# Performance work log

Measured on AMD Instinct MI355X. Metric: run time of the kernel, lower is better.

The kernel has to match this reference:

```python
import jax, jax.numpy as jnp
import numpy as np

N = 50000          # nodes
E = 640000         # edges (before self-loops)
DIM_FEATS = 128
DIM_H = 32
HEADS1 = 8
NUM_CLASS = 16
NEG_SLOPE_ATT = 0.2   # PyG GATv2Conv default negative_slope
NEG_SLOPE_OUT = 0.01  # F.leaky_relu default


def setup_inputs() -> dict:
    key = jax.random.key(0)
    ks = jax.random.split(key, 12)
    s = 0.1
    x = jax.random.normal(ks[0], (N, DIM_FEATS), dtype=jnp.float32)
    edge_index = jax.random.randint(ks[1], (2, E), 0, N, dtype=jnp.int32)
    # GATv2Conv layer 1: dim_feats -> dim_h per head, 8 heads, concat
    W1l = jax.random.normal(ks[2], (DIM_FEATS, HEADS1 * DIM_H), dtype=jnp.float32) * s
    W1r = jax.random.normal(ks[3], (DIM_FEATS, HEADS1 * DIM_H), dtype=jnp.float32) * s
    att1 = jax.random.normal(ks[4], (HEADS1, DIM_H), dtype=jnp.float32) * s
    b1 = jnp.zeros((HEADS1 * DIM_H,), dtype=jnp.float32)
    # GATv2Conv layer 2: 256 -> num_class, 1 head, concat=False
    W2l = jax.random.normal(ks[5], (HEADS1 * DIM_H, NUM_CLASS), dtype=jnp.float32) * s
    W2r = jax.random.normal(ks[6], (HEADS1 * DIM_H, NUM_CLASS), dtype=jnp.float32) * s
    att2 = jax.random.normal(ks[7], (1, NUM_CLASS), dtype=jnp.float32) * s
    b2 = jnp.zeros((NUM_CLASS,), dtype=jnp.float32)
    return {"x": x, "edge_index": edge_index, "W1l": W1l, "W1r": W1r,
            "att1": att1, "b1": b1, "W2l": W2l, "W2r": W2r,
            "att2": att2, "b2": b2}


def _segment_softmax(scores, seg, num_segments):
    # scores: [E, H], seg: [E] destination node ids
    m = jax.ops.segment_max(scores, seg, num_segments=num_segments)  # [N, H]
    e = jnp.exp(scores - m[seg])
    denom = jax.ops.segment_sum(e, seg, num_segments=num_segments)   # [N, H]
    return e / (denom[seg] + 1e-16)


def _gatv2_layer(x, src, dst, Wl, Wr, att, bias, heads, out_ch, concat):
    n = x.shape[0]
    xl = (x @ Wl).reshape(n, heads, out_ch)  # source transform
    xr = (x @ Wr).reshape(n, heads, out_ch)  # target transform
    # per-edge GATv2 score: a^T LeakyReLU(xl[j] + xr[i])
    e = jax.nn.leaky_relu(xl[src] + xr[dst], negative_slope=NEG_SLOPE_ATT)  # [E,H,F]
    alpha = jnp.einsum('ehf,hf->eh', e, att)                                # [E,H]
    alpha = _segment_softmax(alpha, dst, n)
    msg = xl[src] * alpha[:, :, None]                                       # [E,H,F]
    out = jax.ops.segment_sum(msg, dst, num_segments=n)                     # [N,H,F]
    out = out.reshape(n, heads * out_ch) if concat else out.mean(axis=1)
    return out + bias


def reference(x, edge_index, W1l, W1r, att1, b1, W2l, W2r, att2, b2):
    # add_self_loops=True (PyG GATv2Conv default)
    loop = jnp.arange(N, dtype=edge_index.dtype)
    src = jnp.concatenate([edge_index[0], loop])
    dst = jnp.concatenate([edge_index[1], loop])
    # eval mode: all dropouts are identity
    h = _gatv2_layer(x, src, dst, W1l, W1r, att1, b1, HEADS1, DIM_H, concat=True)
    h = jax.nn.elu(h)
    h = _gatv2_layer(h, src, dst, W2l, W2r, att2, b2, 1, NUM_CLASS, concat=False)
    return jax.nn.leaky_relu(h, negative_slope=NEG_SLOPE_OUT)
```

## Files before the change

kernel.cpp:

```cpp
#include <hip/hip_runtime.h>
#include <math.h>

#define NN 50000
#define E0 640000
#define ET 690000
#define F1 128
#define D1 256
#define C2 16
#define NB 196
#define MPAD 50048
#define PADK 136
#define LOG2E 1.4426950408889634f
#define NBK1 782

typedef _Float16 f16x8 __attribute__((ext_vector_type(8)));
typedef _Float16 h2 __attribute__((ext_vector_type(2)));
typedef __attribute__((ext_vector_type(4))) float f32x4;

__device__ __forceinline__ unsigned short f2h(float f) {
  union { _Float16 h; unsigned short u; } c;
  c.h = (_Float16)f;
  return c.u;
}
__device__ __forceinline__ float h2f(unsigned short u) {
  union { unsigned short u; _Float16 h; } c; c.u = u; return (float)c.h;
}
__device__ __forceinline__ h2 u2h2(unsigned u) {
  union { unsigned u; h2 h; } c; c.u = u; return c.h;
}
__device__ __forceinline__ unsigned h22u(h2 h) {
  union { h2 h; unsigned u; } c; c.h = h; return c.u;
}

__global__ __launch_bounds__(256) void k_prep(
    const float* __restrict__ Wl, const float* __restrict__ Wr,
    const float* __restrict__ W2l, const float* __restrict__ W2r,
    const int* __restrict__ ei,
    unsigned short* __restrict__ wt, unsigned short* __restrict__ wt2,
    int* __restrict__ deg) {
  const int b = blockIdx.x;
  if (b < 256) {
    int tid = b * 256 + threadIdx.x;
    int n = tid >> 7, k = tid & 127;
    float v = (n < 256) ? Wl[k * 256 + n] : Wr[k * 256 + (n - 256)];
    wt[tid] = f2h(v);
  } else if (b < 288) {
    int tid = (b - 256) * 256 + threadIdx.x;
    int n = tid >> 8, k = tid & 255;
    float v = (n < 16) ? W2l[k * 16 + n] : W2r[k * 16 + (n - 16)];
    wt2[tid] = f2h(v);
  } else {
    int e = (b - 288) * 256 + threadIdx.x;
    if (e >= ET) return;
    int d = (e < E0) ? ei[E0 + e] : (e - E0);
    atomicAdd(&deg[d], 1);
  }
}

__global__ __launch_bounds__(256) void k_gemm1m(
    const float* __restrict__ x, const unsigned short* __restrict__ wt,
    unsigned short* __restrict__ xlh, unsigned short* __restrict__ xrh) {
  __shared__ unsigned short Al[128 * PADK];
  __shared__ unsigned short Bl[128 * PADK];
  const int t = threadIdx.x;
  const int m0 = blockIdx.x * 128;
  const int n0 = blockIdx.y * 128;
  {
    const int r = t >> 4;
    const int c = (t & 15) * 8;
#pragma unroll
    for (int p = 0; p < 8; ++p) {
      const int row = r + p * 16;
      const int rg = m0 + row;
      const float* xp = &x[(size_t)(rg < NN ? rg : NN - 1) * F1 + c];
      float4 lo = *(const float4*)xp;
      float4 hi = *(const float4*)(xp + 4);
      h2 q0 = h2{(_Float16)lo.x, (_Float16)lo.y};
      h2 q1 = h2{(_Float16)lo.z, (_Float16)lo.w};
      h2 q2 = h2{(_Float16)hi.x, (_Float16)hi.y};
      h2 q3 = h2{(_Float16)hi.z, (_Float16)hi.w};
      uint4 st; st.x = h22u(q0); st.y = h22u(q1); st.z = h22u(q2); st.w = h22u(q3);
      *(uint4*)&Al[row * PADK + c] = st;
      *(float4*)&Bl[row * PADK + c] = *(const float4*)&wt[(size_t)(n0 + row) * F1 + c];
    }
  }
  __syncthreads();
  const int wave = t >> 6, lane = t & 63;
  const int mw = (wave >> 1) * 64, nw = (wave & 1) * 64;
  const int fr = lane & 15, fq = lane >> 4;
  f32x4 acc[4][4] = {};
#pragma unroll
  for (int ks = 0; ks < 4; ++ks) {
    const int ko = ks * 32 + fq * 8;
    f16x8 a[4], b[4];
#pragma unroll
    for (int i = 0; i < 4; ++i)
      a[i] = *(const f16x8*)&Al[(mw + i * 16 + fr) * PADK + ko];
#pragma unroll
    for (int j = 0; j < 4; ++j)
      b[j] = *(const f16x8*)&Bl[(nw + j * 16 + fr) * PADK + ko];
#pragma unroll
    for (int i = 0; i < 4; ++i)
#pragma unroll
      for (int j = 0; j < 4; ++j)
        acc[i][j] = __builtin_amdgcn_mfma_f32_16x16x32_f16(a[i], b[j], acc[i][j], 0, 0, 0);
  }
  unsigned short* outp = (n0 < 256) ? xlh : xrh;
  const int cb = (n0 & 255) + nw + fr;
#pragma unroll
  for (int j = 0; j < 4; ++j) {
    const int col = cb + j * 16;
    const int head = col >> 5, f = col & 31;
    unsigned short* hp = outp + (size_t)head * NN * 32 + f;
#pragma unroll
    for (int i = 0; i < 4; ++i) {
      const int gm0 = m0 + mw + i * 16 + fq * 4;
#pragma unroll
      for (int r = 0; r < 4; ++r) {
        const int gm = gm0 + r;
        if (gm < NN) hp[(size_t)gm * 32] = f2h(acc[i][j][r]);
      }
    }
  }
}

__global__ __launch_bounds__(256) void k_scan_part(const int* __restrict__ deg,
                                                   int* __restrict__ part) {
  int i = blockIdx.x * 256 + threadIdx.x;
  int v = (i < NN) ? deg[i] : 0;
  v += __shfl_xor(v, 1);  v += __shfl_xor(v, 2);  v += __shfl_xor(v, 4);
  v += __shfl_xor(v, 8);  v += __shfl_xor(v, 16); v += __shfl_xor(v, 32);
  __shared__ int w[4];
  if ((threadIdx.x & 63) == 0) w[threadIdx.x >> 6] = v;
  __syncthreads();
  if (threadIdx.x == 0) part[blockIdx.x] = w[0] + w[1] + w[2] + w[3];
}

__global__ __launch_bounds__(256) void k_scan_apply(int* __restrict__ deg,
                                                    const int* __restrict__ part,
                                                    int* __restrict__ offs) {
  __shared__ int lds[256];
  __shared__ int red[4];
  const int b = blockIdx.x, t = threadIdx.x;
  const int i = b * 256 + t;
  int v = (i < NN) ? deg[i] : 0;
  lds[t] = v;
  int pp = 0;
  for (int j = t; j < b; j += 256) pp += part[j];
  pp += __shfl_xor(pp, 1);  pp += __shfl_xor(pp, 2);  pp += __shfl_xor(pp, 4);
  pp += __shfl_xor(pp, 8);  pp += __shfl_xor(pp, 16); pp += __shfl_xor(pp, 32);
  if ((t & 63) == 0) red[t >> 6] = pp;
  __syncthreads();
  const int prefix = red[0] + red[1] + red[2] + red[3];
  for (int off = 1; off < 256; off <<= 1) {
    int u = (t >= off) ? lds[t - off] : 0;
    __syncthreads();
    lds[t] += u;
    __syncthreads();
  }
  int excl = prefix + lds[t] - v;
  if (i < NN) { offs[i] = excl; deg[i] = excl; }
  if (b == NB - 1 && t == 255) offs[NN] = prefix + lds[255];
}

__global__ void k_scatter(const int* __restrict__ ei, int* __restrict__ cur,
                          unsigned short* __restrict__ csr) {
  int e = blockIdx.x * 256 + threadIdx.x;
  if (e >= ET) return;
  int s, d;
  if (e < E0) { s = ei[e]; d = ei[E0 + e]; } else { s = d = e - E0; }
  int pos = atomicAdd(&cur[d], 1);
  csr[pos] = (unsigned short)s;
}

__global__ __launch_bounds__(256) void k_agg1(
    const unsigned short* __restrict__ xlh, const unsigned short* __restrict__ xrh,
    unsigned short* __restrict__ hb,
    const int* __restrict__ offs, const unsigned short* __restrict__ csr,
    const float* __restrict__ att, const float* __restrict__ b1) {
  const int b = blockIdx.x;
  const int head = b & 7;
  const int wave = threadIdx.x >> 6;
  const int lane = threadIdx.x & 63;
  const int g = lane >> 2;
  const int j4 = lane & 3;
  const int n = (b >> 3) * 64 + wave * 16 + g;
  const bool valid = n < NN;
  const int colh = j4 * 8;
  const int col = head * 32 + colh;
  const unsigned short* xlhead = xlh + (size_t)head * NN * 32;

  const int nc = valid ? n : 0;
  const uint4 xru = *(const uint4*)&xrh[((size_t)head * NN + nc) * 32 + colh];
  h2 xr2[4];
  xr2[0] = u2h2(xru.x); xr2[1] = u2h2(xru.y);
  xr2[2] = u2h2(xru.z); xr2[3] = u2h2(xru.w);
  float at8[8];
  *(float4*)&at8[0] = *(const float4*)&att[col];
  *(float4*)&at8[4] = *(const float4*)&att[col + 4];
  h2 ath6[4], ath4[4];
#pragma unroll
  for (int j = 0; j < 4; ++j) {
    ath6[j] = h2{(_Float16)(at8[2 * j] * (0.6f * LOG2E)),
                 (_Float16)(at8[2 * j + 1] * (0.6f * LOG2E))};
    ath4[j] = h2{(_Float16)(at8[2 * j] * (0.4f * LOG2E)),
                 (_Float16)(at8[2 * j + 1] * (0.4f * LOG2E))};
  }
  float l = 0.f;
  h2 acc2[4] = {h2{0, 0}, h2{0, 0}, h2{0, 0}, h2{0, 0}};
  const int beg = valid ? offs[n] : 0;
  const int fin = valid ? offs[n + 1] : 0;

  auto score = [&](const h2* xh) -> float {
    float cv = 0.f, ca = 0.f;
#pragma unroll
    for (int j = 0; j < 4; ++j) {
      h2 v = xh[j] + xr2[j];
      h2 a = u2h2(h22u(v) & 0x7FFF7FFFu);
      cv = __builtin_amdgcn_fdot2(v, ath6[j], cv, false);
      ca = __builtin_amdgcn_fdot2(a, ath4[j], ca, false);
    }
    float c = cv + ca;
    c += __shfl_xor(c, 1);
    c += __shfl_xor(c, 2);
    return c;
  };

  int idx = beg;
  for (; idx + 1 < fin; idx += 2) {
    const int s0 = csr[idx], s1 = csr[idx + 1];
    const uint4 w0 = *(const uint4*)&xlhead[(size_t)s0 * 32 + colh];
    const uint4 w1 = *(const uint4*)&xlhead[(size_t)s1 * 32 + colh];
    h2 xh0[4], xh1[4];
    xh0[0] = u2h2(w0.x); xh0[1] = u2h2(w0.y); xh0[2] = u2h2(w0.z); xh0[3] = u2h2(w0.w);
    xh1[0] = u2h2(w1.x); xh1[1] = u2h2(w1.y); xh1[2] = u2h2(w1.z); xh1[3] = u2h2(w1.w);
    const float c0 = score(xh0);
    const float c1 = score(xh1);
    const float p0 = exp2f(c0), p1 = exp2f(c1);
    l += p0 + p1;
    const _Float16 p0h = (_Float16)p0, p1h = (_Float16)p1;
    const h2 p02 = h2{p0h, p0h}, p12 = h2{p1h, p1h};
#pragma unroll
    for (int j = 0; j < 4; ++j) acc2[j] += p02 * xh0[j] + p12 * xh1[j];
  }
  if (idx < fin) {
    const int s0 = csr[idx];
    const uint4 w0 = *(const uint4*)&xlhead[(size_t)s0 * 32 + colh];
    h2 xh0[4];
    xh0[0] = u2h2(w0.x); xh0[1] = u2h2(w0.y); xh0[2] = u2h2(w0.z); xh0[3] = u2h2(w0.w);
    const float c0 = score(xh0);
    const float p0 = exp2f(c0);
    l += p0;
    const _Float16 p0h = (_Float16)p0;
    const h2 p02 = h2{p0h, p0h};
#pragma unroll
    for (int j = 0; j < 4; ++j) acc2[j] += p02 * xh0[j];
  }
  if (valid) {
    const float rl = 1.f / (l + 1e-16f);
    float b8[8], o[8];
    *(float4*)&b8[0] = *(const float4*)&b1[col];
    *(float4*)&b8[4] = *(const float4*)&b1[col + 4];
#pragma unroll
    for (int j = 0; j < 4; ++j) {
      o[2 * j]     = (float)acc2[j][0] * rl + b8[2 * j];
      o[2 * j + 1] = (float)acc2[j][1] * rl + b8[2 * j + 1];
    }
#pragma unroll
    for (int k = 0; k < 8; ++k) o[k] = o[k] > 0.f ? o[k] : expm1f(o[k]);
    ushort4 p;
    p.x = f2h(o[0]); p.y = f2h(o[1]); p.z = f2h(o[2]); p.w = f2h(o[3]);
    ushort4 q;
    q.x = f2h(o[4]); q.y = f2h(o[5]); q.z = f2h(o[6]); q.w = f2h(o[7]);
    uint4 packed;
    packed.x = *(unsigned*)&p.x; packed.y = *(unsigned*)&p.z;
    packed.z = *(unsigned*)&q.x; packed.w = *(unsigned*)&q.z;
    *(uint4*)&hb[(size_t)n * D1 + col] = packed;
  }
}

__global__ __launch_bounds__(256) void k_gemm2m(
    const unsigned short* __restrict__ hb, const unsigned short* __restrict__ wt2,
    unsigned short* __restrict__ h2lh, float* __restrict__ h2r) {
  const int t = threadIdx.x;
  const int wave = t >> 6, lane = t & 63;
  const int fr = lane & 15, fq = lane >> 4;
  const int m0 = blockIdx.x * 128 + wave * 32;
  f32x4 acc[2][2] = {};
#pragma unroll
  for (int ks = 0; ks < 8; ++ks) {
    const int ko = ks * 32 + fq * 8;
    f16x8 a[2], b[2];
#pragma unroll
    for (int i = 0; i < 2; ++i) {
      int row = m0 + i * 16 + fr; if (row >= NN) row = NN - 1;
      a[i] = *(const f16x8*)&hb[(size_t)row * D1 + ko];
    }
#pragma unroll
    for (int j = 0; j < 2; ++j)
      b[j] = *(const f16x8*)&wt2[(j * 16 + fr) * 256 + ko];
#pragma unroll
    for (int i = 0; i < 2; ++i)
#pragma unroll
      for (int j = 0; j < 2; ++j)
        acc[i][j] = __builtin_amdgcn_mfma_f32_16x16x32_f16(a[i], b[j], acc[i][j], 0, 0, 0);
  }
#pragma unroll
  for (int i = 0; i < 2; ++i) {
    const int gm0 = m0 + i * 16 + fq * 4;
#pragma unroll
    for (int r = 0; r < 4; ++r) {
      const int gm = gm0 + r;
      if (gm < NN) {
        h2lh[(size_t)gm * C2 + fr] = f2h(acc[i][0][r]);
        h2r[(size_t)gm * C2 + fr] = acc[i][1][r];
      }
    }
  }
}

__global__ __launch_bounds__(256) void k_agg2(
    const unsigned short* __restrict__ h2lh, const float* __restrict__ h2r,
    const int* __restrict__ offs, const unsigned short* __restrict__ csr,
    const float* __restrict__ att2, const float* __restrict__ b2,
    float* __restrict__ out) {
  const int wave = threadIdx.x >> 6;
  const int lane = threadIdx.x & 63;
  const int n = blockIdx.x * 4 + wave;
  if (n >= NN) return;
  const int c = lane & 15, g = lane >> 4;
  const float xr_v = h2r[(size_t)n * C2 + c];
  const float att_v = att2[c] * LOG2E;
  float l = 0.f, acc = 0.f;
  const int beg = offs[n], fin = offs[n + 1];
  for (int idx = beg + g; idx < fin; idx += 4) {
    int s = csr[idx];
    float xlv = h2f(h2lh[(size_t)s * C2 + c]);
    float v = xlv + xr_v;
    v = fmaxf(v, 0.2f * v);
    float sc0 = v * att_v;
    sc0 += __shfl_xor(sc0, 1);
    sc0 += __shfl_xor(sc0, 2);
    sc0 += __shfl_xor(sc0, 4);
    sc0 += __shfl_xor(sc0, 8);
    float p = exp2f(sc0);
    l += p;
    acc = fmaf(p, xlv, acc);
  }
  l += __shfl_xor(l, 16);   l += __shfl_xor(l, 32);
  acc += __shfl_xor(acc, 16); acc += __shfl_xor(acc, 32);
  float o = acc / (l + 1e-16f) + b2[c];
  o = o > 0.f ? o : 0.01f * o;
  if (lane < 16) out[(size_t)n * C2 + c] = o;
}

extern "C" void kernel_launch(void* const* d_in, const int* in_sizes, int n_in,
                              void* d_out, int out_size, void* d_ws, size_t ws_size,
                              hipStream_t stream) {
  const float* x    = (const float*)d_in[0];
  const int*   ei   = (const int*)d_in[1];
  const float* W1l  = (const float*)d_in[2];
  const float* W1r  = (const float*)d_in[3];
  const float* att1 = (const float*)d_in[4];
  const float* b1   = (const float*)d_in[5];
  const float* W2l  = (const float*)d_in[6];
  const float* W2r  = (const float*)d_in[7];
  const float* att2 = (const float*)d_in[8];
  const float* b2   = (const float*)d_in[9];
  float* out = (float*)d_out;

  unsigned short* xlh = (unsigned short*)d_ws;
  unsigned short* xrh = xlh + (size_t)NN * D1;
  unsigned short* hb  = xrh + (size_t)NN * D1;
  int* deg  = (int*)(hb + (size_t)NN * D1);
  int* part = deg + NN;
  int* offs = part + NB;
  unsigned short* csr = (unsigned short*)(offs + NN + 1);
  unsigned short* wt  = csr + ET + 2;
  unsigned short* wt2 = wt + 512 * F1;
  unsigned short* h2lh = xlh;
  float* h2r = (float*)(h2lh + (size_t)NN * C2);

  hipMemsetAsync(deg, 0, NN * sizeof(int), stream);
  k_prep<<<288 + (ET + 255) / 256, 256, 0, stream>>>(
      W1l, W1r, W2l, W2r, ei, wt, wt2, deg);
  k_gemm1m<<<dim3(MPAD / 128, 4), 256, 0, stream>>>(x, wt, xlh, xrh);
  k_scan_part<<<NB, 256, 0, stream>>>(deg, part);
  k_scan_apply<<<NB, 256, 0, stream>>>(deg, part, offs);
  k_scatter<<<(ET + 255) / 256, 256, 0, stream>>>(ei, deg, csr);
  k_agg1<<<NBK1 * 8, 256, 0, stream>>>(xlh, xrh, hb, offs, csr, att1, b1);
  k_gemm2m<<<(NN + 127) / 128, 256, 0, stream>>>(hb, wt2, h2lh, h2r);
  k_agg2<<<NN / 4, 256, 0, stream>>>(h2lh, h2r, offs, csr, att2, b2, out);
}
```

Measured before the change: 270.2 us.

## Load x tile once per block across all output chunks; merge scan kernels

The first GEMM now uses 64-row blocks that convert the x tile to fp16 once and then loop over all four 128-column weight chunks. Before, each x tile was reloaded and reconverted by four separate blocks. The two-kernel degree scan is also merged into one kernel, where each block sums all earlier degrees directly and writes cursors to a separate array. This removes one launch, but later blocks repeat a growing prefix reduction, and the GEMM now has fewer blocks, each doing more serial work.

```diff
diff --git a/kernel.cpp b/kernel.cpp
--- a/kernel.cpp
+++ b/kernel.cpp
@@ -60,85 +60,79 @@
 __global__ __launch_bounds__(256) void k_gemm1m(
     const float* __restrict__ x, const unsigned short* __restrict__ wt,
     unsigned short* __restrict__ xlh, unsigned short* __restrict__ xrh) {
-  __shared__ unsigned short Al[128 * PADK];
+  __shared__ unsigned short Al[64 * PADK];
   __shared__ unsigned short Bl[128 * PADK];
   const int t = threadIdx.x;
-  const int m0 = blockIdx.x * 128;
-  const int n0 = blockIdx.y * 128;
-  {
-    const int r = t >> 4;
-    const int c = (t & 15) * 8;
+  const int m0 = blockIdx.x * 64;
+  const int r = t >> 4;
+  const int c = (t & 15) * 8;
+#pragma unroll
+  for (int p = 0; p < 4; ++p) {
+    const int row = r + p * 16;
+    const int rg = m0 + row;
+    const float* xp = &x[(size_t)(rg < NN ? rg : NN - 1) * F1 + c];
+    float4 lo = *(const float4*)xp;
+    float4 hi = *(const float4*)(xp + 4);
+    uint4 st;
+    st.x = h22u(h2{(_Float16)lo.x, (_Float16)lo.y});
+    st.y = h22u(h2{(_Float16)lo.z, (_Float16)lo.w});
+    st.z = h22u(h2{(_Float16)hi.x, (_Float16)hi.y});
+    st.w = h22u(h2{(_Float16)hi.z, (_Float16)hi.w});
+    *(uint4*)&Al[row * PADK + c] = st;
+  }
+  const int wave = t >> 6, lane = t & 63;
+  const int mw = (wave >> 1) * 32, nw = (wave & 1) * 64;
+  const int fr = lane & 15, fq = lane >> 4;
+#pragma unroll
+  for (int chunk = 0; chunk < 4; ++chunk) {
+    const int n0 = chunk * 128;
+    __syncthreads();
 #pragma unroll
     for (int p = 0; p < 8; ++p) {
       const int row = r + p * 16;
-      const int rg = m0 + row;
-      const float* xp = &x[(size_t)(rg < NN ? rg : NN - 1) * F1 + c];
-      float4 lo = *(const float4*)xp;
-      float4 hi = *(const float4*)(xp + 4);
-      h2 q0 = h2{(_Float16)lo.x, (_Float16)lo.y};
-      h2 q1 = h2{(_Float16)lo.z, (_Float16)lo.w};
-      h2 q2 = h2{(_Float16)hi.x, (_Float16)hi.y};
-      h2 q3 = h2{(_Float16)hi.z, (_Float16)hi.w};
-      uint4 st; st.x = h22u(q0); st.y = h22u(q1); st.z = h22u(q2); st.w = h22u(q3);
-      *(uint4*)&Al[row * PADK + c] = st;
       *(float4*)&Bl[row * PADK + c] = *(const float4*)&wt[(size_t)(n0 + row) * F1 + c];
     }
-  }
-  __syncthreads();
-  const int wave = t >> 6, lane = t & 63;
-  const int mw = (wave >> 1) * 64, nw = (wave & 1) * 64;
-  const int fr = lane & 15, fq = lane >> 4;
-  f32x4 acc[4][4] = {};
-#pragma unroll
-  for (int ks = 0; ks < 4; ++ks) {
-    const int ko = ks * 32 + fq * 8;
-    f16x8 a[4], b[4];
-#pragma unroll
-    for (int i = 0; i < 4; ++i)
-      a[i] = *(const f16x8*)&Al[(mw + i * 16 + fr) * PADK + ko];
-#pragma unroll
-    for (int j = 0; j < 4; ++j)
-      b[j] = *(const f16x8*)&Bl[(nw + j * 16 + fr) * PADK + ko];
-#pragma unroll
-    for (int i = 0; i < 4; ++i)
+    __syncthreads();
+    f32x4 acc[2][4] = {};
+#pragma unroll
+    for (int ks = 0; ks < 4; ++ks) {
+      const int ko = ks * 32 + fq * 8;
+      f16x8 a[2], b[4];
+#pragma unroll
+      for (int i = 0; i < 2; ++i)
+        a[i] = *(const f16x8*)&Al[(mw + i * 16 + fr) * PADK + ko];
 #pragma unroll
       for (int j = 0; j < 4; ++j)
-        acc[i][j] = __builtin_amdgcn_mfma_f32_16x16x32_f16(a[i], b[j], acc[i][j], 0, 0, 0);
-  }
-  unsigned short* outp = (n0 < 256) ? xlh : xrh;
-  const int cb = (n0 & 255) + nw + fr;
-#pragma unroll
-  for (int j = 0; j < 4; ++j) {
-    const int col = cb + j * 16;
-    const int head = col >> 5, f = col & 31;
-    unsigned short* hp = outp + (size_t)head * NN * 32 + f;
-#pragma unroll
-    for (int i = 0; i < 4; ++i) {
-      const int gm0 = m0 + mw + i * 16 + fq * 4;
-#pragma unroll
-      for (int r = 0; r < 4; ++r) {
-        const int gm = gm0 + r;
-        if (gm < NN) hp[(size_t)gm * 32] = f2h(acc[i][j][r]);
+        b[j] = *(const f16x8*)&Bl[(nw + j * 16 + fr) * PADK + ko];
+#pragma unroll
+      for (int i = 0; i < 2; ++i)
+#pragma unroll
+        for (int j = 0; j < 4; ++j)
+          acc[i][j] = __builtin_amdgcn_mfma_f32_16x16x32_f16(a[i], b[j], acc[i][j], 0, 0, 0);
+    }
+    unsigned short* outp = (n0 < 256) ? xlh : xrh;
+    const int cb = (n0 & 255) + nw + fr;
+#pragma unroll
+    for (int j = 0; j < 4; ++j) {
+      const int col = cb + j * 16;
+      const int head = col >> 5, f = col & 31;
+      unsigned short* hp = outp + (size_t)head * NN * 32 + f;
+#pragma unroll
+      for (int i = 0; i < 2; ++i) {
+        const int gm0 = m0 + mw + i * 16 + fq * 4;
+#pragma unroll
+        for (int rr = 0; rr < 4; ++rr) {
+          const int gm = gm0 + rr;
+          if (gm < NN) hp[(size_t)gm * 32] = f2h(acc[i][j][rr]);
+        }
       }
     }
   }
 }
 
-__global__ __launch_bounds__(256) void k_scan_part(const int* __restrict__ deg,
-                                                   int* __restrict__ part) {
-  int i = blockIdx.x * 256 + threadIdx.x;
-  int v = (i < NN) ? deg[i] : 0;
-  v += __shfl_xor(v, 1);  v += __shfl_xor(v, 2);  v += __shfl_xor(v, 4);
-  v += __shfl_xor(v, 8);  v += __shfl_xor(v, 16); v += __shfl_xor(v, 32);
-  __shared__ int w[4];
-  if ((threadIdx.x & 63) == 0) w[threadIdx.x >> 6] = v;
-  __syncthreads();
-  if (threadIdx.x == 0) part[blockIdx.x] = w[0] + w[1] + w[2] + w[3];
-}
-
-__global__ __launch_bounds__(256) void k_scan_apply(int* __restrict__ deg,
-                                                    const int* __restrict__ part,
-                                                    int* __restrict__ offs) {
+__global__ __launch_bounds__(256) void k_scan(const int* __restrict__ deg,
+                                              int* __restrict__ offs,
+                                              int* __restrict__ cur) {
   __shared__ int lds[256];
   __shared__ int red[4];
   const int b = blockIdx.x, t = threadIdx.x;
@@ -146,7 +140,8 @@
   int v = (i < NN) ? deg[i] : 0;
   lds[t] = v;
   int pp = 0;
-  for (int j = t; j < b; j += 256) pp += part[j];
+  const int lim = b * 256;
+  for (int j = t; j < lim; j += 256) pp += deg[j];
   pp += __shfl_xor(pp, 1);  pp += __shfl_xor(pp, 2);  pp += __shfl_xor(pp, 4);
   pp += __shfl_xor(pp, 8);  pp += __shfl_xor(pp, 16); pp += __shfl_xor(pp, 32);
   if ((t & 63) == 0) red[t >> 6] = pp;
@@ -159,7 +154,7 @@
     __syncthreads();
   }
   int excl = prefix + lds[t] - v;
-  if (i < NN) { offs[i] = excl; deg[i] = excl; }
+  if (i < NN) { offs[i] = excl; cur[i] = excl; }
   if (b == NB - 1 && t == 255) offs[NN] = prefix + lds[255];
 }
 
@@ -373,8 +368,8 @@
   unsigned short* xrh = xlh + (size_t)NN * D1;
   unsigned short* hb  = xrh + (size_t)NN * D1;
   int* deg  = (int*)(hb + (size_t)NN * D1);
-  int* part = deg + NN;
-  int* offs = part + NB;
+  int* cur  = deg + NN;
+  int* offs = cur + NN;
   unsigned short* csr = (unsigned short*)(offs + NN + 1);
   unsigned short* wt  = csr + ET + 2;
   unsigned short* wt2 = wt + 512 * F1;
@@ -384,10 +379,9 @@
   hipMemsetAsync(deg, 0, NN * sizeof(int), stream);
   k_prep<<<288 + (ET + 255) / 256, 256, 0, stream>>>(
       W1l, W1r, W2l, W2r, ei, wt, wt2, deg);
-  k_gemm1m<<<dim3(MPAD / 128, 4), 256, 0, stream>>>(x, wt, xlh, xrh);
-  k_scan_part<<<NB, 256, 0, stream>>>(deg, part);
-  k_scan_apply<<<NB, 256, 0, stream>>>(deg, part, offs);
-  k_scatter<<<(ET + 255) / 256, 256, 0, stream>>>(ei, deg, csr);
+  k_gemm1m<<<MPAD / 64, 256, 0, stream>>>(x, wt, xlh, xrh);
+  k_scan<<<NB, 256, 0, stream>>>(deg, offs, cur);
+  k_scatter<<<(ET + 255) / 256, 256, 0, stream>>>(ei, cur, csr);
   k_agg1<<<NBK1 * 8, 256, 0, stream>>>(xlh, xrh, hb, offs, csr, att1, b1);
   k_gemm2m<<<(NN + 127) / 128, 256, 0, stream>>>(hb, wt2, h2lh, h2r);
   k_agg2<<<NN / 4, 256, 0, stream>>>(h2lh, h2r, offs, csr, att2, b2, out);
```

Result: slower. 289.7 us (+7.2%).

## Sort nodes by in-degree via counting sort to balance agg1 work

Applied to the files above, without the earlier changes.

Builds a degree histogram during the scan, prefix-sums it into bucket offsets, and scatters node ids into a degree-sorted permutation. The first aggregation kernel then processes nodes in that order, so the 16 nodes sharing a wave have similar edge counts and less divergence. The cost is an extra atomic histogram, a 512-entry scan, a permutation pass, and scattered writes and reads of xr and hb for each node.

```diff
diff --git a/kernel.cpp b/kernel.cpp
--- a/kernel.cpp
+++ b/kernel.cpp
@@ -8,6 +8,7 @@
 #define D1 256
 #define C2 16
 #define NB 196
+#define EB 2696
 #define MPAD 50048
 #define PADK 136
 #define LOG2E 1.4426950408889634f
@@ -75,11 +76,11 @@
       const float* xp = &x[(size_t)(rg < NN ? rg : NN - 1) * F1 + c];
       float4 lo = *(const float4*)xp;
       float4 hi = *(const float4*)(xp + 4);
-      h2 q0 = h2{(_Float16)lo.x, (_Float16)lo.y};
-      h2 q1 = h2{(_Float16)lo.z, (_Float16)lo.w};
-      h2 q2 = h2{(_Float16)hi.x, (_Float16)hi.y};
-      h2 q3 = h2{(_Float16)hi.z, (_Float16)hi.w};
-      uint4 st; st.x = h22u(q0); st.y = h22u(q1); st.z = h22u(q2); st.w = h22u(q3);
+      uint4 st;
+      st.x = h22u(h2{(_Float16)lo.x, (_Float16)lo.y});
+      st.y = h22u(h2{(_Float16)lo.z, (_Float16)lo.w});
+      st.z = h22u(h2{(_Float16)hi.x, (_Float16)hi.y});
+      st.w = h22u(h2{(_Float16)hi.z, (_Float16)hi.w});
       *(uint4*)&Al[row * PADK + c] = st;
       *(float4*)&Bl[row * PADK + c] = *(const float4*)&wt[(size_t)(n0 + row) * F1 + c];
     }
@@ -125,22 +126,27 @@
 }
 
 __global__ __launch_bounds__(256) void k_scan_part(const int* __restrict__ deg,
-                                                   int* __restrict__ part) {
+                                                   int* __restrict__ part,
+                                                   int* __restrict__ degcnt) {
   int i = blockIdx.x * 256 + threadIdx.x;
   int v = (i < NN) ? deg[i] : 0;
-  v += __shfl_xor(v, 1);  v += __shfl_xor(v, 2);  v += __shfl_xor(v, 4);
-  v += __shfl_xor(v, 8);  v += __shfl_xor(v, 16); v += __shfl_xor(v, 32);
+  if (i < NN) atomicAdd(&degcnt[v < 511 ? v : 511], 1);
+  int s = v;
+  s += __shfl_xor(s, 1);  s += __shfl_xor(s, 2);  s += __shfl_xor(s, 4);
+  s += __shfl_xor(s, 8);  s += __shfl_xor(s, 16); s += __shfl_xor(s, 32);
   __shared__ int w[4];
-  if ((threadIdx.x & 63) == 0) w[threadIdx.x >> 6] = v;
+  if ((threadIdx.x & 63) == 0) w[threadIdx.x >> 6] = s;
   __syncthreads();
   if (threadIdx.x == 0) part[blockIdx.x] = w[0] + w[1] + w[2] + w[3];
 }
 
 __global__ __launch_bounds__(256) void k_scan_apply(int* __restrict__ deg,
                                                     const int* __restrict__ part,
-                                                    int* __restrict__ offs) {
+                                                    int* __restrict__ offs,
+                                                    int* __restrict__ degcnt) {
   __shared__ int lds[256];
   __shared__ int red[4];
+  __shared__ int bl[512];
   const int b = blockIdx.x, t = threadIdx.x;
   const int i = b * 256 + t;
   int v = (i < NN) ? deg[i] : 0;
@@ -161,22 +167,49 @@
   int excl = prefix + lds[t] - v;
   if (i < NN) { offs[i] = excl; deg[i] = excl; }
   if (b == NB - 1 && t == 255) offs[NN] = prefix + lds[255];
+  if (b == 0) {
+    const int o0 = degcnt[t], o1 = degcnt[t + 256];
+    bl[t] = o0; bl[t + 256] = o1;
+    __syncthreads();
+    for (int off = 1; off < 512; off <<= 1) {
+      int a0 = (t >= off) ? bl[t - off] : 0;
+      int a1 = (t + 256 >= off) ? bl[t + 256 - off] : 0;
+      __syncthreads();
+      bl[t] += a0; bl[t + 256] += a1;
+      __syncthreads();
+    }
+    degcnt[t] = bl[t] - o0;
+    degcnt[t + 256] = bl[t + 256] - o1;
+  }
 }
 
 __global__ void k_scatter(const int* __restrict__ ei, int* __restrict__ cur,
-                          unsigned short* __restrict__ csr) {
-  int e = blockIdx.x * 256 + threadIdx.x;
-  if (e >= ET) return;
-  int s, d;
-  if (e < E0) { s = ei[e]; d = ei[E0 + e]; } else { s = d = e - E0; }
-  int pos = atomicAdd(&cur[d], 1);
-  csr[pos] = (unsigned short)s;
+                          const int* __restrict__ offs, int* __restrict__ degcnt,
+                          unsigned short* __restrict__ csr,
+                          unsigned short* __restrict__ perm) {
+  const int b = blockIdx.x;
+  if (b < EB) {
+    int e = b * 256 + threadIdx.x;
+    if (e >= ET) return;
+    int s, d;
+    if (e < E0) { s = ei[e]; d = ei[E0 + e]; } else { s = d = e - E0; }
+    int pos = atomicAdd(&cur[d], 1);
+    csr[pos] = (unsigned short)s;
+  } else {
+    int i = (b - EB) * 256 + threadIdx.x;
+    if (i >= NN) return;
+    int v = offs[i + 1] - offs[i];
+    int bucket = v < 511 ? v : 511;
+    int pos = atomicAdd(&degcnt[bucket], 1);
+    perm[pos] = (unsigned short)i;
+  }
 }
 
 __global__ __launch_bounds__(256) void k_agg1(
     const unsigned short* __restrict__ xlh, const unsigned short* __restrict__ xrh,
     unsigned short* __restrict__ hb,
     const int* __restrict__ offs, const unsigned short* __restrict__ csr,
+    const unsigned short* __restrict__ perm,
     const float* __restrict__ att, const float* __restrict__ b1) {
   const int b = blockIdx.x;
   const int head = b & 7;
@@ -184,14 +217,14 @@
   const int lane = threadIdx.x & 63;
   const int g = lane >> 2;
   const int j4 = lane & 3;
-  const int n = (b >> 3) * 64 + wave * 16 + g;
-  const bool valid = n < NN;
+  const int pos = (b >> 3) * 64 + wave * 16 + g;
+  const bool valid = pos < NN;
+  const int n = valid ? (int)perm[pos] : 0;
   const int colh = j4 * 8;
   const int col = head * 32 + colh;
   const unsigned short* xlhead = xlh + (size_t)head * NN * 32;
 
-  const int nc = valid ? n : 0;
-  const uint4 xru = *(const uint4*)&xrh[((size_t)head * NN + nc) * 32 + colh];
+  const uint4 xru = *(const uint4*)&xrh[((size_t)head * NN + n) * 32 + colh];
   h2 xr2[4];
   xr2[0] = u2h2(xru.x); xr2[1] = u2h2(xru.y);
   xr2[2] = u2h2(xru.z); xr2[3] = u2h2(xru.w);
@@ -374,21 +407,23 @@
   unsigned short* hb  = xrh + (size_t)NN * D1;
   int* deg  = (int*)(hb + (size_t)NN * D1);
   int* part = deg + NN;
-  int* offs = part + NB;
-  unsigned short* csr = (unsigned short*)(offs + NN + 1);
+  int* degcnt = part + NB;
+  int* offs = degcnt + 512;
+  unsigned short* perm = (unsigned short*)(offs + NN + 1);
+  unsigned short* csr = perm + NN + 2;
   unsigned short* wt  = csr + ET + 2;
   unsigned short* wt2 = wt + 512 * F1;
   unsigned short* h2lh = xlh;
   float* h2r = (float*)(h2lh + (size_t)NN * C2);
 
-  hipMemsetAsync(deg, 0, NN * sizeof(int), stream);
+  hipMemsetAsync(deg, 0, (NN + NB + 512) * sizeof(int), stream);
   k_prep<<<288 + (ET + 255) / 256, 256, 0, stream>>>(
       W1l, W1r, W2l, W2r, ei, wt, wt2, deg);
   k_gemm1m<<<dim3(MPAD / 128, 4), 256, 0, stream>>>(x, wt, xlh, xrh);
-  k_scan_part<<<NB, 256, 0, stream>>>(deg, part);
-  k_scan_apply<<<NB, 256, 0, stream>>>(deg, part, offs);
-  k_scatter<<<(ET + 255) / 256, 256, 0, stream>>>(ei, deg, csr);
-  k_agg1<<<NBK1 * 8, 256, 0, stream>>>(xlh, xrh, hb, offs, csr, att1, b1);
+  k_scan_part<<<NB, 256, 0, stream>>>(deg, part, degcnt);
+  k_scan_apply<<<NB, 256, 0, stream>>>(deg, part, offs, degcnt);
+  k_scatter<<<EB + NB, 256, 0, stream>>>(ei, deg, offs, degcnt, csr, perm);
+  k_agg1<<<NBK1 * 8, 256, 0, stream>>>(xlh, xrh, hb, offs, csr, perm, att1, b1);
   k_gemm2m<<<(NN + 127) / 128, 256, 0, stream>>>(hb, wt2, h2lh, h2r);
   k_agg2<<<NN / 4, 256, 0, stream>>>(h2lh, h2r, offs, csr, att2, b2, out);
 }
```

Result: slower. 544.2 us (+101.4%).
